# Kernel optimization log

Measured on AMD Instinct MI355X. Metric: run time of the kernel, lower is better.

## Reference

```python
import jax, jax.numpy as jnp
import numpy as np

N = 100000          # nodes
E = 1_600_000       # edges (before self loops)
IN = 128            # in_channels
HID = 64            # hidden
HEADS = 4
EPS = 1e-5          # BatchNorm eps
NEG_SLOPE = 0.2     # GATConv leaky_relu slope


def setup_inputs() -> dict:
    key = jax.random.key(0)
    ks = jax.random.split(key, 16)
    he = lambda fan: (2.0 / fan) ** 0.5  # kaiming-normal scale
    d = {
        "x": jax.random.normal(ks[0], (N, IN), jnp.float32),
        "edge_index": jax.random.randint(ks[1], (2, E), 0, N, dtype=jnp.int64),
        "root_index": 0,
        "W1": jax.random.normal(ks[2], (IN, HEADS * HID), jnp.float32) * he(IN),
        "att_src1": jax.random.normal(ks[3], (HEADS, HID), jnp.float32) * 0.1,
        "att_dst1": jax.random.normal(ks[4], (HEADS, HID), jnp.float32) * 0.1,
        "b1": jnp.zeros((HEADS * HID,), jnp.float32),
        "W2": jax.random.normal(ks[5], (HEADS * HID, HID), jnp.float32) * he(HEADS * HID),
        "att_src2": jax.random.normal(ks[6], (1, HID), jnp.float32) * 0.1,
        "att_dst2": jax.random.normal(ks[7], (1, HID), jnp.float32) * 0.1,
        "b2": jnp.zeros((HID,), jnp.float32),
        "bn1_g": jnp.ones((HEADS * HID,), jnp.float32),
        "bn1_b": jnp.zeros((HEADS * HID,), jnp.float32),
        "bn1_m": jnp.zeros((HEADS * HID,), jnp.float32),
        "bn1_v": jnp.ones((HEADS * HID,), jnp.float32),
        "bn2_g": jnp.ones((HID,), jnp.float32),
        "bn2_b": jnp.zeros((HID,), jnp.float32),
        "bn2_m": jnp.zeros((HID,), jnp.float32),
        "bn2_v": jnp.ones((HID,), jnp.float32),
        "cg1_w": jax.random.normal(ks[8], (3 * HID, 64), jnp.float32) * he(3 * HID),
        "cg1_b": jnp.zeros((64,), jnp.float32),
        "cbn_g": jnp.ones((64,), jnp.float32),
        "cbn_b": jnp.zeros((64,), jnp.float32),
        "cbn_m": jnp.zeros((64,), jnp.float32),
        "cbn_v": jnp.ones((64,), jnp.float32),
        "cg2_w": jax.random.normal(ks[9], (64, 32), jnp.float32) * he(64),
        "cg2_b": jnp.zeros((32,), jnp.float32),
        "cg3_w": jax.random.normal(ks[10], (32, 1), jnp.float32) * he(32),
        "cg3_b": jnp.zeros((1,), jnp.float32),
    }
    return d


def _bn_eval(x, g, b, m, v):
    return (x - m) * jax.lax.rsqrt(v + EPS) * g + b


def _gat_conv(x, src, dst, W, att_src, att_dst, bias, heads, out_ch, concat):
    """PyG GATConv (eval mode, self loops already in src/dst)."""
    n = x.shape[0]
    h = (x @ W).reshape(n, heads, out_ch)                # [N,H,C]
    a_src = jnp.einsum('nhc,hc->nh', h, att_src)         # [N,H]
    a_dst = jnp.einsum('nhc,hc->nh', h, att_dst)
    e = jax.nn.leaky_relu(a_src[src] + a_dst[dst], NEG_SLOPE)   # [Etot,H]
    seg_max = jax.ops.segment_max(e, dst, num_segments=n)
    ex = jnp.exp(e - seg_max[dst])
    denom = jax.ops.segment_sum(ex, dst, num_segments=n)
    alpha = ex / (denom[dst] + 1e-16)                    # [Etot,H]
    msg = h[src] * alpha[:, :, None]                     # [Etot,H,C]
    out = jax.ops.segment_sum(msg, dst, num_segments=n)  # [N,H,C]
    if concat:
        return out.reshape(n, heads * out_ch) + bias
    return out.mean(axis=1) + bias


def reference(x, edge_index, root_index, W1, att_src1, att_dst1, b1,
              W2, att_src2, att_dst2, b2,
              bn1_g, bn1_b, bn1_m, bn1_v, bn2_g, bn2_b, bn2_m, bn2_v,
              cg1_w, cg1_b, cbn_g, cbn_b, cbn_m, cbn_v,
              cg2_w, cg2_b, cg3_w, cg3_b):
    n = x.shape[0]
    # add self loops (PyG GATConv default)
    loop = jnp.arange(n, dtype=edge_index.dtype)
    src = jnp.concatenate([edge_index[0], loop])
    dst = jnp.concatenate([edge_index[1], loop])

    h = _gat_conv(x, src, dst, W1, att_src1, att_dst1, b1, HEADS, HID, True)
    h = jax.nn.elu(_bn_eval(h, bn1_g, bn1_b, bn1_m, bn1_v))
    h = _gat_conv(h, src, dst, W2, att_src2, att_dst2, b2, 1, HID, False)
    node_emb = jax.nn.elu(_bn_eval(h, bn2_g, bn2_b, bn2_m, bn2_v))  # [N,HID]

    mean_emb = node_emb.mean(axis=0, keepdims=True)      # [1,HID]
    max_emb = node_emb.max(axis=0, keepdims=True)        # [1,HID]
    safe_root = min(root_index, n - 1)
    root_emb = node_emb[safe_root][None, :]              # single graph path
    g = jnp.concatenate([mean_emb, max_emb, root_emb], axis=-1)  # [1,3*HID]

    g = jax.nn.relu(_bn_eval(g @ cg1_w + cg1_b, cbn_g, cbn_b, cbn_m, cbn_v))
    g = jax.nn.relu(g @ cg2_w + cg2_b)
    logit = (g @ cg3_w + cg3_b).squeeze(-1)              # [1]
    return logit
```

## Files before the change

kernel.cpp:

```cpp
#include <hip/hip_runtime.h>

#define N_NODES 100000
#define N_EDGES 1600000
#define ETOT    1700000
#define IN_CH   128
#define C1      256
#define HID     64
#define BN_EPS  1e-5f
#define SLOPE   0.2f
#define NCHUNK  98
#define DEG_PH  8
#define DEG_PHN 12500
#define FILL_PH 12
#define FILL_PHN 8334

typedef __attribute__((ext_vector_type(8))) short s16x8;
typedef __attribute__((ext_vector_type(4))) float f32x4;
#define MFMA16(a, b, c) __builtin_amdgcn_mfma_f32_16x16x32_bf16(a, b, c, 0, 0, 0)

__device__ __forceinline__ float leaky(float x) { return fmaxf(x, SLOPE * x); }
__device__ __forceinline__ float elu_f(float x) { return x > 0.f ? x : __expf(x) - 1.f; }
__device__ __forceinline__ unsigned short f2bf(float f) {
  unsigned int b = __float_as_uint(f);
  return (unsigned short)((b + 0x7FFFu + ((b >> 16) & 1u)) >> 16);
}
__device__ __forceinline__ float bf2f(unsigned short u) {
  return __uint_as_float((unsigned int)u << 16);
}

__global__ void __launch_bounds__(256) k_init_deg(int* __restrict__ deg) {
  int n = blockIdx.x * 256 + threadIdx.x;
  if (n < N_NODES) deg[n] = 1;
}

__global__ void __launch_bounds__(256) k_deg_ph(const int* __restrict__ edge, int* __restrict__ deg) {
  int bpp = (N_EDGES + 1023) >> 10;
  int ph = blockIdx.x / bpp;
  int lo = ph * DEG_PHN, hi = lo + DEG_PHN;
  int i0 = (blockIdx.x % bpp) * 1024 + threadIdx.x * 4;
  if (i0 >= N_EDGES) return;
  if (i0 + 3 < N_EDGES) {
    int4 dv = *(const int4*)(edge + N_EDGES + i0);
    if (dv.x >= lo && dv.x < hi) atomicAdd(&deg[dv.x], 1);
    if (dv.y >= lo && dv.y < hi) atomicAdd(&deg[dv.y], 1);
    if (dv.z >= lo && dv.z < hi) atomicAdd(&deg[dv.z], 1);
    if (dv.w >= lo && dv.w < hi) atomicAdd(&deg[dv.w], 1);
  } else {
    for (int j = 0; j < 4 && i0 + j < N_EDGES; j++) {
      int d = edge[N_EDGES + i0 + j];
      if (d >= lo && d < hi) atomicAdd(&deg[d], 1);
    }
  }
}

__global__ void __launch_bounds__(256) k_scan_part(const int* __restrict__ deg, int* __restrict__ part) {
  __shared__ int ls[256];
  int t = threadIdx.x;
  int base = blockIdx.x * 1024 + t * 4;
  int s = 0;
#pragma unroll
  for (int j = 0; j < 4; j++) if (base + j < N_NODES) s += deg[base + j];
  ls[t] = s;
  __syncthreads();
  for (int off = 128; off >= 1; off >>= 1) {
    if (t < off) ls[t] += ls[t + off];
    __syncthreads();
  }
  if (t == 0) part[blockIdx.x] = ls[0];
}

__global__ void k_scan_top(int* __restrict__ part, int* __restrict__ row_ptr) {
  if (threadIdx.x == 0 && blockIdx.x == 0) {
    int run = 0;
    for (int i = 0; i < NCHUNK; i++) { int t = part[i]; part[i] = run; run += t; }
    row_ptr[N_NODES] = run;
  }
}

__global__ void __launch_bounds__(256) k_scan_down(const int* __restrict__ deg, const int* __restrict__ part,
                                                   int* __restrict__ row_ptr, int* __restrict__ cursor) {
  __shared__ int ls[256];
  int t = threadIdx.x;
  int base = blockIdx.x * 1024 + t * 4;
  int v[4];
#pragma unroll
  for (int j = 0; j < 4; j++) v[j] = (base + j < N_NODES) ? deg[base + j] : 0;
  int tsum = v[0] + v[1] + v[2] + v[3];
  ls[t] = tsum;
  __syncthreads();
  for (int off = 1; off < 256; off <<= 1) {
    int add = (t >= off) ? ls[t - off] : 0;
    __syncthreads();
    ls[t] += add;
    __syncthreads();
  }
  int excl = ls[t] - tsum + part[blockIdx.x];
#pragma unroll
  for (int j = 0; j < 4; j++) {
    int idx = base + j;
    if (idx < N_NODES) { row_ptr[idx] = excl; cursor[idx] = excl; }
    excl += v[j];
  }
}

__global__ void __launch_bounds__(256) k_fill_ph(const int* __restrict__ edge, int* __restrict__ cursor,
                                                 const float* __restrict__ aS, const float* __restrict__ aD,
                                                 int* __restrict__ col, float* __restrict__ w1) {
  int bpp = (ETOT + 255) >> 8;
  int ph = blockIdx.x / bpp;
  int lo = ph * FILL_PHN, hi = lo + FILL_PHN;
  int i = (blockIdx.x % bpp) * 256 + threadIdx.x;
  if (i >= ETOT) return;
  int d = (i < N_EDGES) ? edge[N_EDGES + i] : (i - N_EDGES);
  if (d < lo || d >= hi) return;
  int s = (i < N_EDGES) ? edge[i] : d;
  int pos = atomicAdd(&cursor[d], 1);
  col[pos] = s;
  float4 as4 = *(const float4*)(aS + (size_t)s * 4);
  float4 ad4 = *(const float4*)(aD + (size_t)d * 4);
  float4 w;
  w.x = __expf(fminf(leaky(as4.x + ad4.x), 80.f));
  w.y = __expf(fminf(leaky(as4.y + ad4.y), 80.f));
  w.z = __expf(fminf(leaky(as4.z + ad4.z), 80.f));
  w.w = __expf(fminf(leaky(as4.w + ad4.w), 80.f));
  *(float4*)(w1 + (size_t)pos * 4) = w;
}

__global__ void __launch_bounds__(256) k_prep(const float* __restrict__ W1, const float* __restrict__ W2,
                                              unsigned short* __restrict__ W1T, unsigned short* __restrict__ W2T) {
  int i = blockIdx.x * 256 + threadIdx.x;
  if (i < IN_CH * C1) {
    int k = i >> 8, c = i & 255;
    W1T[c * IN_CH + k] = f2bf(W1[i]);
  }
  if (i < C1 * HID) {
    int k = i >> 6, c = i & 63;
    W2T[c * C1 + k] = f2bf(W2[i]);
  }
}

__global__ void __launch_bounds__(256) k_gemm1(const float* __restrict__ x, const unsigned short* __restrict__ W1T,
                                               const float* __restrict__ attS, const float* __restrict__ attD,
                                               unsigned short* __restrict__ h1b, float* __restrict__ aS,
                                               float* __restrict__ aD) {
  __shared__ unsigned short As[64][IN_CH + 8];
  int tid = threadIdx.x;
  int w = tid >> 6, lane = tid & 63;
  int l15 = lane & 15, l4 = lane >> 4;
  int row0 = blockIdx.x * 64;
#pragma unroll
  for (int it = 0; it < 8; it++) {
    int idx = tid + it * 256;
    int r = idx >> 5;
    int k4 = (idx & 31) * 4;
    int gr = row0 + r; if (gr >= N_NODES) gr = N_NODES - 1;
    float4 v = *(const float4*)(x + (size_t)gr * IN_CH + k4);
    ushort4 bvec;
    bvec.x = f2bf(v.x); bvec.y = f2bf(v.y); bvec.z = f2bf(v.z); bvec.w = f2bf(v.w);
    *(ushort4*)&As[r][k4] = bvec;
  }
  __syncthreads();
  f32x4 acc[4][4];
#pragma unroll
  for (int mf = 0; mf < 4; mf++)
#pragma unroll
    for (int cf = 0; cf < 4; cf++) acc[mf][cf] = (f32x4){0.f, 0.f, 0.f, 0.f};
#pragma unroll
  for (int ks = 0; ks < 4; ks++) {
    int koff = ks * 32 + l4 * 8;
    s16x8 a[4];
#pragma unroll
    for (int mf = 0; mf < 4; mf++) a[mf] = *(const s16x8*)&As[mf * 16 + l15][koff];
#pragma unroll
    for (int cf = 0; cf < 4; cf++) {
      s16x8 b = *(const s16x8*)(W1T + (size_t)(w * 64 + cf * 16 + l15) * IN_CH + koff);
#pragma unroll
      for (int mf = 0; mf < 4; mf++) acc[mf][cf] = MFMA16(a[mf], b, acc[mf][cf]);
    }
  }
  float as_c[4], ad_c[4];
#pragma unroll
  for (int cf = 0; cf < 4; cf++) {
    as_c[cf] = attS[w * HID + cf * 16 + l15];
    ad_c[cf] = attD[w * HID + cf * 16 + l15];
  }
#pragma unroll
  for (int mf = 0; mf < 4; mf++) {
#pragma unroll
    for (int reg = 0; reg < 4; reg++) {
      int gr = row0 + mf * 16 + l4 * 4 + reg;
      bool ok = gr < N_NODES;
      float s = 0.f, dd = 0.f;
#pragma unroll
      for (int cf = 0; cf < 4; cf++) {
        float v = acc[mf][cf][reg];
        if (ok) h1b[(size_t)gr * C1 + w * 64 + cf * 16 + l15] = f2bf(v);
        s += v * as_c[cf];
        dd += v * ad_c[cf];
      }
#pragma unroll
      for (int m = 1; m <= 8; m <<= 1) { s += __shfl_xor(s, m, 64); dd += __shfl_xor(dd, m, 64); }
      if (ok && l15 == 0) {
        aS[(size_t)gr * 4 + w] = s;
        aD[(size_t)gr * 4 + w] = dd;
      }
    }
  }
}

__global__ void __launch_bounds__(256) k_agg1(const int* __restrict__ row_ptr, const int* __restrict__ col,
                                              const float* __restrict__ w1,
                                              const unsigned short* __restrict__ h1b, const float* __restrict__ b1,
                                              const float* __restrict__ g1, const float* __restrict__ be1,
                                              const float* __restrict__ m1, const float* __restrict__ v1,
                                              unsigned short* __restrict__ hmb) {
  int wave = threadIdx.x >> 6;
  int lane = threadIdx.x & 63;
  int d = blockIdx.x * 4 + wave;
  if (d >= N_NODES) return;
  int head = lane >> 4;
  int s0 = row_ptr[d], s1 = row_ptr[d + 1];
  int s1m1 = s1 - 1;
  float denom = 0.f;
  float4 acc = {0.f, 0.f, 0.f, 0.f};
  int c0 = lane * 4;
  for (int base = s0; base < s1; base += 8) {
    int left = s1 - base;
    int idx = base + (lane & 7); if (idx > s1m1) idx = s1m1;
    int cv = col[idx];
    int sid[8];
#pragma unroll
    for (int j = 0; j < 8; j++) sid[j] = __builtin_amdgcn_readfirstlane(__shfl(cv, j));
    float wv[8];
#pragma unroll
    for (int j = 0; j < 8; j++) {
      int wi = base + j; if (wi > s1m1) wi = s1m1;
      float wl = w1[(size_t)wi * 4 + head];
      wv[j] = (j < left) ? wl : 0.f;
    }
    ushort4 h[8];
#pragma unroll
    for (int j = 0; j < 8; j++) h[j] = *(const ushort4*)(h1b + ((size_t)sid[j] << 8) + c0);
#pragma unroll
    for (int j = 0; j < 8; j++) {
      denom += wv[j];
      acc.x += wv[j] * bf2f(h[j].x);
      acc.y += wv[j] * bf2f(h[j].y);
      acc.z += wv[j] * bf2f(h[j].z);
      acc.w += wv[j] * bf2f(h[j].w);
    }
  }
  float inv = 1.f / (denom + 1e-16f);
  float4 bb = *(const float4*)(b1 + c0);
  float4 gg = *(const float4*)(g1 + c0);
  float4 be = *(const float4*)(be1 + c0);
  float4 mm = *(const float4*)(m1 + c0);
  float4 vv = *(const float4*)(v1 + c0);
  ushort4 o;
  o.x = f2bf(elu_f((acc.x * inv + bb.x - mm.x) * rsqrtf(vv.x + BN_EPS) * gg.x + be.x));
  o.y = f2bf(elu_f((acc.y * inv + bb.y - mm.y) * rsqrtf(vv.y + BN_EPS) * gg.y + be.y));
  o.z = f2bf(elu_f((acc.z * inv + bb.z - mm.z) * rsqrtf(vv.z + BN_EPS) * gg.z + be.z));
  o.w = f2bf(elu_f((acc.w * inv + bb.w - mm.w) * rsqrtf(vv.w + BN_EPS) * gg.w + be.w));
  *(ushort4*)(hmb + (size_t)d * C1 + c0) = o;
}

__global__ void __launch_bounds__(256) k_gemm2(const unsigned short* __restrict__ hmb, const unsigned short* __restrict__ W2T,
                                               const float* __restrict__ attS, const float* __restrict__ attD,
                                               unsigned short* __restrict__ h2b, float* __restrict__ aS,
                                               float* __restrict__ aD) {
  __shared__ unsigned short As[64][C1 + 8];
  int tid = threadIdx.x;
  int w = tid >> 6, lane = tid & 63;
  int l15 = lane & 15, l4 = lane >> 4;
  int row0 = blockIdx.x * 64;
#pragma unroll
  for (int it = 0; it < 8; it++) {
    int idx = tid + it * 256;
    int r = idx >> 5;
    int k8 = (idx & 31) * 8;
    int gr = row0 + r; if (gr >= N_NODES) gr = N_NODES - 1;
    *(uint4*)&As[r][k8] = *(const uint4*)(hmb + (size_t)gr * C1 + k8);
  }
  __syncthreads();
  f32x4 acc[4];
#pragma unroll
  for (int cf = 0; cf < 4; cf++) acc[cf] = (f32x4){0.f, 0.f, 0.f, 0.f};
#pragma unroll
  for (int ks = 0; ks < 8; ks++) {
    int koff = ks * 32 + l4 * 8;
    s16x8 a = *(const s16x8*)&As[w * 16 + l15][koff];
#pragma unroll
    for (int cf = 0; cf < 4; cf++) {
      s16x8 b = *(const s16x8*)(W2T + (size_t)(cf * 16 + l15) * C1 + koff);
      acc[cf] = MFMA16(a, b, acc[cf]);
    }
  }
  float as_c[4], ad_c[4];
#pragma unroll
  for (int cf = 0; cf < 4; cf++) {
    as_c[cf] = attS[cf * 16 + l15];
    ad_c[cf] = attD[cf * 16 + l15];
  }
#pragma unroll
  for (int reg = 0; reg < 4; reg++) {
    int gr = row0 + w * 16 + l4 * 4 + reg;
    bool ok = gr < N_NODES;
    float s = 0.f, dd = 0.f;
#pragma unroll
    for (int cf = 0; cf < 4; cf++) {
      float v = acc[cf][reg];
      if (ok) h2b[(size_t)gr * HID + cf * 16 + l15] = f2bf(v);
      s += v * as_c[cf];
      dd += v * ad_c[cf];
    }
#pragma unroll
    for (int m = 1; m <= 8; m <<= 1) { s += __shfl_xor(s, m, 64); dd += __shfl_xor(dd, m, 64); }
    if (ok && l15 == 0) { aS[gr] = s; aD[gr] = dd; }
  }
}

__global__ void __launch_bounds__(256) k_agg2(const int* __restrict__ row_ptr, const int* __restrict__ col,
                                              const float* __restrict__ aS, const float* __restrict__ aD,
                                              const unsigned short* __restrict__ h2b, const float* __restrict__ b2,
                                              const float* __restrict__ g2, const float* __restrict__ be2,
                                              const float* __restrict__ m2, const float* __restrict__ v2,
                                              float* __restrict__ emb) {
  int wave = threadIdx.x >> 6;
  int lane = threadIdx.x & 63;
  int d = blockIdx.x * 4 + wave;
  if (d >= N_NODES) return;
  float ad = aD[d];
  int s0 = row_ptr[d], s1 = row_ptr[d + 1];
  int s1m1 = s1 - 1;
  float denom = 0.f, acc = 0.f;
  for (int base = s0; base < s1; base += 8) {
    int left = s1 - base;
    int idx = base + (lane & 7); if (idx > s1m1) idx = s1m1;
    int cv = col[idx];
    int sid[8];
#pragma unroll
    for (int j = 0; j < 8; j++) sid[j] = __builtin_amdgcn_readfirstlane(__shfl(cv, j));
    float e[8];
#pragma unroll
    for (int j = 0; j < 8; j++) e[j] = aS[sid[j]];
    unsigned short h[8];
#pragma unroll
    for (int j = 0; j < 8; j++) h[j] = h2b[((size_t)sid[j] << 6) + lane];
    float wv[8];
#pragma unroll
    for (int j = 0; j < 8; j++) {
      float wl = __expf(fminf(leaky(e[j] + ad), 80.f));
      wv[j] = (j < left) ? wl : 0.f;
    }
#pragma unroll
    for (int j = 0; j < 8; j++) {
      denom += wv[j];
      acc += wv[j] * bf2f(h[j]);
    }
  }
  float o = acc / (denom + 1e-16f) + b2[lane];
  o = (o - m2[lane]) * rsqrtf(v2[lane] + BN_EPS) * g2[lane] + be2[lane];
  emb[(size_t)d * HID + lane] = elu_f(o);
}

__global__ void __launch_bounds__(256) k_pool(const float* __restrict__ emb, float* __restrict__ psum,
                                              float* __restrict__ pmax) {
  __shared__ float ss[4][64], sm[4][64];
  int t = threadIdx.x;
  int c = t & 63, rg = t >> 6;
  float s = 0.f, m = -INFINITY;
  for (int n = blockIdx.x * 4 + rg; n < N_NODES; n += gridDim.x * 4) {
    float v = emb[(size_t)n * HID + c];
    s += v; m = fmaxf(m, v);
  }
  ss[rg][c] = s; sm[rg][c] = m;
  __syncthreads();
  if (t < 64) {
    psum[blockIdx.x * 64 + t] = ss[0][t] + ss[1][t] + ss[2][t] + ss[3][t];
    pmax[blockIdx.x * 64 + t] = fmaxf(fmaxf(sm[0][t], sm[1][t]), fmaxf(sm[2][t], sm[3][t]));
  }
}

__global__ void __launch_bounds__(256) k_final(const float* __restrict__ psum, const float* __restrict__ pmax,
                                               const float* __restrict__ emb, const int* __restrict__ rootp,
                                               const float* __restrict__ cg1w, const float* __restrict__ cg1b,
                                               const float* __restrict__ cbng, const float* __restrict__ cbnb,
                                               const float* __restrict__ cbnm, const float* __restrict__ cbnv,
                                               const float* __restrict__ cg2w, const float* __restrict__ cg2b,
                                               const float* __restrict__ cg3w, const float* __restrict__ cg3b,
                                               float* __restrict__ out) {
  __shared__ float ss[4][64], sm[4][64];
  __shared__ float g[192], t1[64], t2[32];
  int t = threadIdx.x;
  int c = t & 63, q = t >> 6;
  float s = 0.f, m = -INFINITY;
  for (int b = q; b < 256; b += 4) {
    s += psum[b * 64 + c];
    m = fmaxf(m, pmax[b * 64 + c]);
  }
  ss[q][c] = s; sm[q][c] = m;
  __syncthreads();
  if (t < 64) {
    float tot = ss[0][t] + ss[1][t] + ss[2][t] + ss[3][t];
    float mx = fmaxf(fmaxf(sm[0][t], sm[1][t]), fmaxf(sm[2][t], sm[3][t]));
    int root = rootp[0];
    if (root > N_NODES - 1) root = N_NODES - 1;
    if (root < 0) root = 0;
    g[t] = tot / (float)N_NODES;
    g[64 + t] = mx;
    g[128 + t] = emb[(size_t)root * HID + t];
  }
  __syncthreads();
  if (t < 64) {
    float o = cg1b[t];
    for (int i = 0; i < 192; i++) o += g[i] * cg1w[i * 64 + t];
    o = (o - cbnm[t]) * rsqrtf(cbnv[t] + BN_EPS) * cbng[t] + cbnb[t];
    t1[t] = o > 0.f ? o : 0.f;
  }
  __syncthreads();
  if (t < 32) {
    float o = cg2b[t];
    for (int i = 0; i < 64; i++) o += t1[i] * cg2w[i * 32 + t];
    t2[t] = o > 0.f ? o : 0.f;
  }
  __syncthreads();
  if (t == 0) {
    float o = cg3b[0];
    for (int i = 0; i < 32; i++) o += t2[i] * cg3w[i];
    out[0] = o;
  }
}

extern "C" void kernel_launch(void* const* d_in, const int* in_sizes, int n_in,
                              void* d_out, int out_size, void* d_ws, size_t ws_size,
                              hipStream_t stream) {
  const float* x     = (const float*)d_in[0];
  const int*   edge  = (const int*)d_in[1];
  const int*   root  = (const int*)d_in[2];
  const float* W1    = (const float*)d_in[3];
  const float* attS1 = (const float*)d_in[4];
  const float* attD1 = (const float*)d_in[5];
  const float* b1    = (const float*)d_in[6];
  const float* W2    = (const float*)d_in[7];
  const float* attS2 = (const float*)d_in[8];
  const float* attD2 = (const float*)d_in[9];
  const float* b2    = (const float*)d_in[10];
  const float* bn1g  = (const float*)d_in[11];
  const float* bn1b  = (const float*)d_in[12];
  const float* bn1m  = (const float*)d_in[13];
  const float* bn1v  = (const float*)d_in[14];
  const float* bn2g  = (const float*)d_in[15];
  const float* bn2b  = (const float*)d_in[16];
  const float* bn2m  = (const float*)d_in[17];
  const float* bn2v  = (const float*)d_in[18];
  const float* cg1w  = (const float*)d_in[19];
  const float* cg1b  = (const float*)d_in[20];
  const float* cbng  = (const float*)d_in[21];
  const float* cbnb  = (const float*)d_in[22];
  const float* cbnm  = (const float*)d_in[23];
  const float* cbnv  = (const float*)d_in[24];
  const float* cg2w  = (const float*)d_in[25];
  const float* cg2b  = (const float*)d_in[26];
  const float* cg3w  = (const float*)d_in[27];
  const float* cg3b  = (const float*)d_in[28];

  char* ws = (char*)d_ws;
  size_t off = 0;
  auto carve = [&](size_t bytes) { char* p = ws + off; off += (bytes + 255) & ~(size_t)255; return p; };
  unsigned short* h1b = (unsigned short*)carve((size_t)N_NODES * C1 * 2);
  unsigned short* hmb = (unsigned short*)carve((size_t)N_NODES * C1 * 2);
  float* aS1     = (float*)carve((size_t)N_NODES * 4 * 4);
  float* aD1     = (float*)carve((size_t)N_NODES * 4 * 4);
  int*   deg     = (int*)  carve((size_t)N_NODES * 4);
  int*   row_ptr = (int*)  carve((size_t)(N_NODES + 1) * 4);
  int*   cursor  = (int*)  carve((size_t)N_NODES * 4);
  int*   col     = (int*)  carve((size_t)ETOT * 4);
  float* w1      = (float*)carve((size_t)ETOT * 4 * 4);
  int*   part    = (int*)  carve(512);
  unsigned short* W1T = (unsigned short*)carve((size_t)IN_CH * C1 * 2);
  unsigned short* W2T = (unsigned short*)carve((size_t)C1 * HID * 2);
  unsigned short* h2b = h1b;
  float* aS2  = (float*)(h1b + (size_t)N_NODES * HID);
  float* aD2  = aS2 + N_NODES;
  float* emb  = (float*)hmb;
  float* psum = emb + (size_t)N_NODES * HID;
  float* pmax = psum + 256 * 64;

  int bpp_deg  = (N_EDGES + 1023) >> 10;
  int bpp_fill = (ETOT + 255) >> 8;
  k_init_deg<<<(N_NODES + 255) / 256, 256, 0, stream>>>(deg);
  k_deg_ph<<<bpp_deg * DEG_PH, 256, 0, stream>>>(edge, deg);
  k_prep<<<(IN_CH * C1 + 255) / 256, 256, 0, stream>>>(W1, W2, W1T, W2T);
  k_gemm1<<<(N_NODES + 63) / 64, 256, 0, stream>>>(x, W1T, attS1, attD1, h1b, aS1, aD1);
  k_scan_part<<<NCHUNK, 256, 0, stream>>>(deg, part);
  k_scan_top<<<1, 64, 0, stream>>>(part, row_ptr);
  k_scan_down<<<NCHUNK, 256, 0, stream>>>(deg, part, row_ptr, cursor);
  k_fill_ph<<<bpp_fill * FILL_PH, 256, 0, stream>>>(edge, cursor, aS1, aD1, col, w1);
  k_agg1<<<(N_NODES + 3) / 4, 256, 0, stream>>>(row_ptr, col, w1, h1b, b1, bn1g, bn1b, bn1m, bn1v, hmb);
  k_gemm2<<<(N_NODES + 63) / 64, 256, 0, stream>>>(hmb, W2T, attS2, attD2, h2b, aS2, aD2);
  k_agg2<<<(N_NODES + 3) / 4, 256, 0, stream>>>(row_ptr, col, aS2, aD2, h2b, b2, bn2g, bn2b, bn2m, bn2v, emb);
  k_pool<<<256, 256, 0, stream>>>(emb, psum, pmax);
  k_final<<<1, 256, 0, stream>>>(psum, pmax, emb, root, cg1w, cg1b, cbng, cbnb, cbnm, cbnv,
                                 cg2w, cg2b, cg3w, cg3b, (float*)d_out);
}
```

Baseline: 507.9 us.

## Fuse layer-1 aggregation with GEMM2 and pooling into agg2

Aggregation for layer 1 now runs 16 nodes per 1024-thread block, stages the BN/ELU output in shared memory, and computes the second projection plus attention logits with MFMA in the same kernel. This removes the 256-wide bf16 intermediate round trip through global memory. Pooling (sum/max via atomics with order-preserving float encoding) and root extraction move into agg2, which drops the k_pool kernel and the emb buffer. The init and prep kernels are also merged. In exchange, only one wave does the small GEMM while 15 wait, and the larger 1024-thread blocks may reduce occupancy.

```diff
diff --git a/kernel.cpp b/kernel.cpp
--- a/kernel.cpp
+++ b/kernel.cpp
@@ -27,10 +27,30 @@
 __device__ __forceinline__ float bf2f(unsigned short u) {
   return __uint_as_float((unsigned int)u << 16);
 }
-
-__global__ void __launch_bounds__(256) k_init_deg(int* __restrict__ deg) {
-  int n = blockIdx.x * 256 + threadIdx.x;
-  if (n < N_NODES) deg[n] = 1;
+__device__ __forceinline__ unsigned int encf(float f) {
+  unsigned int b = __float_as_uint(f);
+  return b ^ ((((int)b >> 31)) | 0x80000000u);
+}
+__device__ __forceinline__ float decf(unsigned int k) {
+  unsigned int b = (k & 0x80000000u) ? (k ^ 0x80000000u) : ~k;
+  return __uint_as_float(b);
+}
+
+__global__ void __launch_bounds__(256) k_prep_init(const float* __restrict__ W1, const float* __restrict__ W2,
+                                                   unsigned short* __restrict__ W1T, unsigned short* __restrict__ W2T,
+                                                   int* __restrict__ deg, float* __restrict__ psum,
+                                                   unsigned int* __restrict__ pmaxenc) {
+  int i = blockIdx.x * 256 + threadIdx.x;
+  if (i < N_NODES) deg[i] = 1;
+  if (i < IN_CH * C1) {
+    int k = i >> 8, c = i & 255;
+    W1T[c * IN_CH + k] = f2bf(W1[i]);
+  }
+  if (i < C1 * HID) {
+    int k = i >> 6, c = i & 63;
+    W2T[c * C1 + k] = f2bf(W2[i]);
+  }
+  if (i < 256 * 64) { psum[i] = 0.f; pmaxenc[i] = 0u; }
 }
 
 __global__ void __launch_bounds__(256) k_deg_ph(const int* __restrict__ edge, int* __restrict__ deg) {
@@ -126,19 +146,6 @@
   *(float4*)(w1 + (size_t)pos * 4) = w;
 }
 
-__global__ void __launch_bounds__(256) k_prep(const float* __restrict__ W1, const float* __restrict__ W2,
-                                              unsigned short* __restrict__ W1T, unsigned short* __restrict__ W2T) {
-  int i = blockIdx.x * 256 + threadIdx.x;
-  if (i < IN_CH * C1) {
-    int k = i >> 8, c = i & 255;
-    W1T[c * IN_CH + k] = f2bf(W1[i]);
-  }
-  if (i < C1 * HID) {
-    int k = i >> 6, c = i & 63;
-    W2T[c * C1 + k] = f2bf(W2[i]);
-  }
-}
-
 __global__ void __launch_bounds__(256) k_gemm1(const float* __restrict__ x, const unsigned short* __restrict__ W1T,
                                                const float* __restrict__ attS, const float* __restrict__ attD,
                                                unsigned short* __restrict__ h1b, float* __restrict__ aS,
@@ -208,16 +215,20 @@
   }
 }
 
-__global__ void __launch_bounds__(256) k_agg1(const int* __restrict__ row_ptr, const int* __restrict__ col,
-                                              const float* __restrict__ w1,
-                                              const unsigned short* __restrict__ h1b, const float* __restrict__ b1,
-                                              const float* __restrict__ g1, const float* __restrict__ be1,
-                                              const float* __restrict__ m1, const float* __restrict__ v1,
-                                              unsigned short* __restrict__ hmb) {
+__global__ void __launch_bounds__(1024) k_agg1g2(const int* __restrict__ row_ptr, const int* __restrict__ col,
+                                                 const float* __restrict__ w1,
+                                                 const unsigned short* __restrict__ h1b, const float* __restrict__ b1,
+                                                 const float* __restrict__ g1, const float* __restrict__ be1,
+                                                 const float* __restrict__ m1, const float* __restrict__ v1,
+                                                 const unsigned short* __restrict__ W2T,
+                                                 const float* __restrict__ attS2, const float* __restrict__ attD2,
+                                                 unsigned short* __restrict__ h2b, float* __restrict__ aS2,
+                                                 float* __restrict__ aD2) {
+  __shared__ unsigned short Hm[16][C1 + 8];
   int wave = threadIdx.x >> 6;
   int lane = threadIdx.x & 63;
-  int d = blockIdx.x * 4 + wave;
-  if (d >= N_NODES) return;
+  int l15 = lane & 15, l4 = lane >> 4;
+  int d = blockIdx.x * 16 + wave;
   int head = lane >> 4;
   int s0 = row_ptr[d], s1 = row_ptr[d + 1];
   int s1m1 = s1 - 1;
@@ -261,61 +272,43 @@
   o.y = f2bf(elu_f((acc.y * inv + bb.y - mm.y) * rsqrtf(vv.y + BN_EPS) * gg.y + be.y));
   o.z = f2bf(elu_f((acc.z * inv + bb.z - mm.z) * rsqrtf(vv.z + BN_EPS) * gg.z + be.z));
   o.w = f2bf(elu_f((acc.w * inv + bb.w - mm.w) * rsqrtf(vv.w + BN_EPS) * gg.w + be.w));
-  *(ushort4*)(hmb + (size_t)d * C1 + c0) = o;
-}
-
-__global__ void __launch_bounds__(256) k_gemm2(const unsigned short* __restrict__ hmb, const unsigned short* __restrict__ W2T,
-                                               const float* __restrict__ attS, const float* __restrict__ attD,
-                                               unsigned short* __restrict__ h2b, float* __restrict__ aS,
-                                               float* __restrict__ aD) {
-  __shared__ unsigned short As[64][C1 + 8];
-  int tid = threadIdx.x;
-  int w = tid >> 6, lane = tid & 63;
-  int l15 = lane & 15, l4 = lane >> 4;
-  int row0 = blockIdx.x * 64;
-#pragma unroll
-  for (int it = 0; it < 8; it++) {
-    int idx = tid + it * 256;
-    int r = idx >> 5;
-    int k8 = (idx & 31) * 8;
-    int gr = row0 + r; if (gr >= N_NODES) gr = N_NODES - 1;
-    *(uint4*)&As[r][k8] = *(const uint4*)(hmb + (size_t)gr * C1 + k8);
-  }
-  __syncthreads();
-  f32x4 acc[4];
-#pragma unroll
-  for (int cf = 0; cf < 4; cf++) acc[cf] = (f32x4){0.f, 0.f, 0.f, 0.f};
-#pragma unroll
-  for (int ks = 0; ks < 8; ks++) {
-    int koff = ks * 32 + l4 * 8;
-    s16x8 a = *(const s16x8*)&As[w * 16 + l15][koff];
+  *(ushort4*)&Hm[wave][c0] = o;
+  __syncthreads();
+  if (wave == 0) {
+    f32x4 acc2[4];
+#pragma unroll
+    for (int cf = 0; cf < 4; cf++) acc2[cf] = (f32x4){0.f, 0.f, 0.f, 0.f};
+#pragma unroll
+    for (int ks = 0; ks < 8; ks++) {
+      int koff = ks * 32 + l4 * 8;
+      s16x8 a = *(const s16x8*)&Hm[l15][koff];
+#pragma unroll
+      for (int cf = 0; cf < 4; cf++) {
+        s16x8 b = *(const s16x8*)(W2T + (size_t)(cf * 16 + l15) * C1 + koff);
+        acc2[cf] = MFMA16(a, b, acc2[cf]);
+      }
+    }
+    float as_c[4], ad_c[4];
 #pragma unroll
     for (int cf = 0; cf < 4; cf++) {
-      s16x8 b = *(const s16x8*)(W2T + (size_t)(cf * 16 + l15) * C1 + koff);
-      acc[cf] = MFMA16(a, b, acc[cf]);
-    }
-  }
-  float as_c[4], ad_c[4];
-#pragma unroll
-  for (int cf = 0; cf < 4; cf++) {
-    as_c[cf] = attS[cf * 16 + l15];
-    ad_c[cf] = attD[cf * 16 + l15];
-  }
-#pragma unroll
-  for (int reg = 0; reg < 4; reg++) {
-    int gr = row0 + w * 16 + l4 * 4 + reg;
-    bool ok = gr < N_NODES;
-    float s = 0.f, dd = 0.f;
-#pragma unroll
-    for (int cf = 0; cf < 4; cf++) {
-      float v = acc[cf][reg];
-      if (ok) h2b[(size_t)gr * HID + cf * 16 + l15] = f2bf(v);
-      s += v * as_c[cf];
-      dd += v * ad_c[cf];
-    }
-#pragma unroll
-    for (int m = 1; m <= 8; m <<= 1) { s += __shfl_xor(s, m, 64); dd += __shfl_xor(dd, m, 64); }
-    if (ok && l15 == 0) { aS[gr] = s; aD[gr] = dd; }
+      as_c[cf] = attS2[cf * 16 + l15];
+      ad_c[cf] = attD2[cf * 16 + l15];
+    }
+#pragma unroll
+    for (int reg = 0; reg < 4; reg++) {
+      int gr = blockIdx.x * 16 + l4 * 4 + reg;
+      float s = 0.f, dd = 0.f;
+#pragma unroll
+      for (int cf = 0; cf < 4; cf++) {
+        float v = acc2[cf][reg];
+        h2b[(size_t)gr * HID + cf * 16 + l15] = f2bf(v);
+        s += v * as_c[cf];
+        dd += v * ad_c[cf];
+      }
+#pragma unroll
+      for (int m = 1; m <= 8; m <<= 1) { s += __shfl_xor(s, m, 64); dd += __shfl_xor(dd, m, 64); }
+      if (l15 == 0) { aS2[gr] = s; aD2[gr] = dd; }
+    }
   }
 }
 
@@ -324,11 +317,12 @@
                                               const unsigned short* __restrict__ h2b, const float* __restrict__ b2,
                                               const float* __restrict__ g2, const float* __restrict__ be2,
                                               const float* __restrict__ m2, const float* __restrict__ v2,
-                                              float* __restrict__ emb) {
+                                              const int* __restrict__ rootp, float* __restrict__ psum,
+                                              unsigned int* __restrict__ pmaxenc, float* __restrict__ root_emb) {
+  __shared__ float ss[4][64], sm[4][64];
   int wave = threadIdx.x >> 6;
   int lane = threadIdx.x & 63;
   int d = blockIdx.x * 4 + wave;
-  if (d >= N_NODES) return;
   float ad = aD[d];
   int s0 = row_ptr[d], s1 = row_ptr[d + 1];
   int s1m1 = s1 - 1;
@@ -360,29 +354,26 @@
   }
   float o = acc / (denom + 1e-16f) + b2[lane];
   o = (o - m2[lane]) * rsqrtf(v2[lane] + BN_EPS) * g2[lane] + be2[lane];
-  emb[(size_t)d * HID + lane] = elu_f(o);
-}
-
-__global__ void __launch_bounds__(256) k_pool(const float* __restrict__ emb, float* __restrict__ psum,
-                                              float* __restrict__ pmax) {
-  __shared__ float ss[4][64], sm[4][64];
-  int t = threadIdx.x;
-  int c = t & 63, rg = t >> 6;
-  float s = 0.f, m = -INFINITY;
-  for (int n = blockIdx.x * 4 + rg; n < N_NODES; n += gridDim.x * 4) {
-    float v = emb[(size_t)n * HID + c];
-    s += v; m = fmaxf(m, v);
-  }
-  ss[rg][c] = s; sm[rg][c] = m;
-  __syncthreads();
-  if (t < 64) {
-    psum[blockIdx.x * 64 + t] = ss[0][t] + ss[1][t] + ss[2][t] + ss[3][t];
-    pmax[blockIdx.x * 64 + t] = fmaxf(fmaxf(sm[0][t], sm[1][t]), fmaxf(sm[2][t], sm[3][t]));
-  }
-}
-
-__global__ void __launch_bounds__(256) k_final(const float* __restrict__ psum, const float* __restrict__ pmax,
-                                               const float* __restrict__ emb, const int* __restrict__ rootp,
+  o = elu_f(o);
+  ss[wave][lane] = o;
+  sm[wave][lane] = o;
+  int root0 = rootp[0];
+  if (root0 > N_NODES - 1) root0 = N_NODES - 1;
+  if (root0 < 0) root0 = 0;
+  if (d == root0) root_emb[lane] = o;
+  __syncthreads();
+  if (threadIdx.x < 64) {
+    int c = threadIdx.x;
+    float s4 = ss[0][c] + ss[1][c] + ss[2][c] + ss[3][c];
+    float m4 = fmaxf(fmaxf(sm[0][c], sm[1][c]), fmaxf(sm[2][c], sm[3][c]));
+    int slot = (blockIdx.x & 255) * 64 + c;
+    atomicAdd(&psum[slot], s4);
+    atomicMax(&pmaxenc[slot], encf(m4));
+  }
+}
+
+__global__ void __launch_bounds__(256) k_final(const float* __restrict__ psum, const unsigned int* __restrict__ pmaxenc,
+                                               const float* __restrict__ root_emb,
                                                const float* __restrict__ cg1w, const float* __restrict__ cg1b,
                                                const float* __restrict__ cbng, const float* __restrict__ cbnb,
                                                const float* __restrict__ cbnm, const float* __restrict__ cbnv,
@@ -396,19 +387,16 @@
   float s = 0.f, m = -INFINITY;
   for (int b = q; b < 256; b += 4) {
     s += psum[b * 64 + c];
-    m = fmaxf(m, pmax[b * 64 + c]);
+    m = fmaxf(m, decf(pmaxenc[b * 64 + c]));
   }
   ss[q][c] = s; sm[q][c] = m;
   __syncthreads();
   if (t < 64) {
     float tot = ss[0][t] + ss[1][t] + ss[2][t] + ss[3][t];
     float mx = fmaxf(fmaxf(sm[0][t], sm[1][t]), fmaxf(sm[2][t], sm[3][t]));
-    int root = rootp[0];
-    if (root > N_NODES - 1) root = N_NODES - 1;
-    if (root < 0) root = 0;
     g[t] = tot / (float)N_NODES;
     g[64 + t] = mx;
-    g[128 + t] = emb[(size_t)root * HID + t];
+    g[128 + t] = root_emb[t];
   }
   __syncthreads();
   if (t < 64) {
@@ -468,38 +456,36 @@
   size_t off = 0;
   auto carve = [&](size_t bytes) { char* p = ws + off; off += (bytes + 255) & ~(size_t)255; return p; };
   unsigned short* h1b = (unsigned short*)carve((size_t)N_NODES * C1 * 2);
-  unsigned short* hmb = (unsigned short*)carve((size_t)N_NODES * C1 * 2);
+  float* w1      = (float*)carve((size_t)ETOT * 4 * 4);
+  unsigned short* h2b = (unsigned short*)carve((size_t)N_NODES * HID * 2);
   float* aS1     = (float*)carve((size_t)N_NODES * 4 * 4);
   float* aD1     = (float*)carve((size_t)N_NODES * 4 * 4);
+  float* aS2     = (float*)carve((size_t)N_NODES * 4);
+  float* aD2     = (float*)carve((size_t)N_NODES * 4);
   int*   deg     = (int*)  carve((size_t)N_NODES * 4);
   int*   row_ptr = (int*)  carve((size_t)(N_NODES + 1) * 4);
   int*   cursor  = (int*)  carve((size_t)N_NODES * 4);
   int*   col     = (int*)  carve((size_t)ETOT * 4);
-  float* w1      = (float*)carve((size_t)ETOT * 4 * 4);
   int*   part    = (int*)  carve(512);
   unsigned short* W1T = (unsigned short*)carve((size_t)IN_CH * C1 * 2);
   unsigned short* W2T = (unsigned short*)carve((size_t)C1 * HID * 2);
-  unsigned short* h2b = h1b;
-  float* aS2  = (float*)(h1b + (size_t)N_NODES * HID);
-  float* aD2  = aS2 + N_NODES;
-  float* emb  = (float*)hmb;
-  float* psum = emb + (size_t)N_NODES * HID;
-  float* pmax = psum + 256 * 64;
+  float* psum    = (float*)carve(256 * 64 * 4);
+  unsigned int* pmaxenc = (unsigned int*)carve(256 * 64 * 4);
+  float* root_emb = (float*)carve(64 * 4);
 
   int bpp_deg  = (N_EDGES + 1023) >> 10;
   int bpp_fill = (ETOT + 255) >> 8;
-  k_init_deg<<<(N_NODES + 255) / 256, 256, 0, stream>>>(deg);
+  k_prep_init<<<(N_NODES + 255) / 256, 256, 0, stream>>>(W1, W2, W1T, W2T, deg, psum, pmaxenc);
   k_deg_ph<<<bpp_deg * DEG_PH, 256, 0, stream>>>(edge, deg);
-  k_prep<<<(IN_CH * C1 + 255) / 256, 256, 0, stream>>>(W1, W2, W1T, W2T);
   k_gemm1<<<(N_NODES + 63) / 64, 256, 0, stream>>>(x, W1T, attS1, attD1, h1b, aS1, aD1);
   k_scan_part<<<NCHUNK, 256, 0, stream>>>(deg, part);
   k_scan_top<<<1, 64, 0, stream>>>(part, row_ptr);
   k_scan_down<<<NCHUNK, 256, 0, stream>>>(deg, part, row_ptr, cursor);
   k_fill_ph<<<bpp_fill * FILL_PH, 256, 0, stream>>>(edge, cursor, aS1, aD1, col, w1);
-  k_agg1<<<(N_NODES + 3) / 4, 256, 0, stream>>>(row_ptr, col, w1, h1b, b1, bn1g, bn1b, bn1m, bn1v, hmb);
-  k_gemm2<<<(N_NODES + 63) / 64, 256, 0, stream>>>(hmb, W2T, attS2, attD2, h2b, aS2, aD2);
-  k_agg2<<<(N_NODES + 3) / 4, 256, 0, stream>>>(row_ptr, col, aS2, aD2, h2b, b2, bn2g, bn2b, bn2m, bn2v, emb);
-  k_pool<<<256, 256, 0, stream>>>(emb, psum, pmax);
-  k_final<<<1, 256, 0, stream>>>(psum, pmax, emb, root, cg1w, cg1b, cbng, cbnb, cbnm, cbnv,
+  k_agg1g2<<<N_NODES / 16, 1024, 0, stream>>>(row_ptr, col, w1, h1b, b1, bn1g, bn1b, bn1m, bn1v,
+                                              W2T, attS2, attD2, h2b, aS2, aD2);
+  k_agg2<<<N_NODES / 4, 256, 0, stream>>>(row_ptr, col, aS2, aD2, h2b, b2, bn2g, bn2b, bn2m, bn2v,
+                                          root, psum, pmaxenc, root_emb);
+  k_final<<<1, 256, 0, stream>>>(psum, pmaxenc, root_emb, cg1w, cg1b, cbng, cbnb, cbnm, cbnv,
                                  cg2w, cg2b, cg3w, cg3b, (float*)d_out);
 }
```

Measured after the change: 507.1 us. About the same (-0.2%).
